# Performance work log

Measured on AMD Instinct MI355X. Metric: run time of the kernel, lower is better.

Reference implementation:

```python
import jax, jax.numpy as jnp
from jax import lax
import numpy as np

D_MODEL = 1024
D_STATE = 64
D_CONV = 4
EXPAND = 2
HEADDIM = 64
D_INNER = EXPAND * D_MODEL          # 2048
NHEADS = D_INNER // HEADDIM         # 32
CHUNK = 64
CONV_DIM = D_INNER + 2 * D_STATE    # 2176
D_IN_PROJ = 2 * D_INNER + 2 * D_STATE + NHEADS  # 4256
B_SZ = 4
SEQLEN = 2048
EPS = 1e-5


def _silu(x):
    return x * jax.nn.sigmoid(x)


def _segsum(x):
    # x: [..., T]; returns [..., T, T] with [i,j] = sum_{j<k<=i} x[k], -inf above diag
    T = x.shape[-1]
    xe = jnp.broadcast_to(x[..., None], x.shape + (T,))
    strict_lower = jnp.tril(jnp.ones((T, T), bool), -1)
    xe = jnp.where(strict_lower, xe, 0.0)
    s = jnp.cumsum(xe, axis=-2)
    lower = jnp.tril(jnp.ones((T, T), bool), 0)
    return jnp.where(lower, s, -jnp.inf)


def setup_inputs() -> dict:
    key = jax.random.key(0)
    ks = jax.random.split(key, 5)
    u = jax.random.normal(ks[0], (B_SZ, SEQLEN, D_MODEL), jnp.float32)
    W_in = jax.random.normal(ks[1], (D_IN_PROJ, D_MODEL), jnp.float32) * 0.02
    conv_w = jax.random.normal(ks[2], (CONV_DIM, 1, D_CONV), jnp.float32) * 0.2  # depthwise kernel
    conv_b = jnp.zeros((CONV_DIM,), jnp.float32)
    dt_bias = jax.random.uniform(ks[3], (NHEADS,), jnp.float32, -1.0, 1.0)
    A_log = jnp.log(jnp.linspace(1.0, float(NHEADS), NHEADS)).astype(jnp.float32)
    D = jnp.ones((NHEADS,), jnp.float32)
    norm_w = jnp.ones((D_INNER,), jnp.float32)
    W_out = jax.random.normal(ks[4], (D_MODEL, D_INNER), jnp.float32) * 0.02
    return dict(u=u, W_in=W_in, conv_w=conv_w, conv_b=conv_b, dt_bias=dt_bias,
                A_log=A_log, D=D, norm_w=norm_w, W_out=W_out)


def reference(u, W_in, conv_w, conv_b, dt_bias, A_log, D, norm_w, W_out):
    b, s, _ = u.shape
    A = -jnp.exp(A_log)                                   # [H]
    zxbcdt = u @ W_in.T                                   # [b,s,D_IN_PROJ]
    z = zxbcdt[..., :D_INNER]
    xBC = zxbcdt[..., D_INNER:D_INNER + CONV_DIM]
    dt = jax.nn.softplus(zxbcdt[..., D_INNER + CONV_DIM:] + dt_bias)  # [b,s,H]

    # causal depthwise conv1d (left pad d_conv-1 == torch pad-both + slice[:s])
    xc = lax.conv_general_dilated(
        xBC.transpose(0, 2, 1), conv_w, window_strides=(1,),
        padding=[(D_CONV - 1, 0)], feature_group_count=CONV_DIM,
        dimension_numbers=('NCH', 'OIH', 'NCH'))
    xBC = _silu(xc.transpose(0, 2, 1) + conv_b)           # [b,s,CONV_DIM]

    x = xBC[..., :D_INNER].reshape(b, s, NHEADS, HEADDIM)
    Bm = xBC[..., D_INNER:D_INNER + D_STATE]              # [b,s,N]
    Cm = xBC[..., D_INNER + D_STATE:]                     # [b,s,N]

    # SSD chunked scan
    nch = s // CHUNK
    xs = (x * dt[..., None]).reshape(b, nch, CHUNK, NHEADS, HEADDIM)
    Ad = (A * dt).reshape(b, nch, CHUNK, NHEADS)
    Br = Bm.reshape(b, nch, CHUNK, D_STATE)
    Cr = Cm.reshape(b, nch, CHUNK, D_STATE)
    A_ch = Ad.transpose(0, 1, 3, 2)                       # [b,c,h,l]
    A_cum = jnp.cumsum(A_ch, axis=-1)
    L = jnp.exp(_segsum(A_ch))                            # [b,c,h,l,l]
    Y_diag = jnp.einsum('bcln,bcsn,bchls,bcshp->bclhp', Cr, Br, L, xs)
    decay_states = jnp.exp(A_cum[..., -1:] - A_cum)       # [b,c,h,l]
    states = jnp.einsum('bchl,bcln,bclhp->bchpn', decay_states, Br, xs)
    init = jnp.zeros((b, 1, NHEADS, HEADDIM, D_STATE), xs.dtype)
    states = jnp.concatenate([init, states], axis=1)      # [b,c+1,h,p,n]
    total_decay = jnp.pad(A_cum[..., -1].transpose(0, 2, 1), ((0, 0), (0, 0), (1, 0)))
    decay_chunk = jnp.exp(_segsum(total_decay))           # [b,h,c+1,c+1]
    new_states = jnp.einsum('bhzc,bchpn->bzhpn', decay_chunk, states)
    states = new_states[:, :-1]                           # [b,c,h,p,n]
    state_decay_out = jnp.exp(A_cum)
    Y_off = jnp.einsum('bcln,bchpn,bchl->bclhp', Cr, states, state_decay_out)
    y = (Y_diag + Y_off).reshape(b, s, NHEADS, HEADDIM)

    y = y + x * D[:, None]
    y = y.reshape(b, s, D_INNER)
    # gated RMSNorm
    y = y * _silu(z)
    y = y * lax.rsqrt(jnp.mean(y * y, axis=-1, keepdims=True) + EPS) * norm_w
    return y @ W_out.T
```

## Files before the change

### kernel.cpp

```cpp
#include <hip/hip_runtime.h>
#include <hip/hip_bf16.h>

#define BSZ 4
#define SEQ 2048
#define DMODEL 1024
#define DINNER 2048
#define DSTATE 64
#define NH 32
#define HD 64
#define CKL 64
#define NCH 32
#define CONVD 2176
#define DPROJ 4256
#define N1 4224
#define MTOT 8192
#define YSTR 72

typedef __hip_bfloat16 bf16;
typedef __attribute__((ext_vector_type(8))) short short8;
typedef __attribute__((ext_vector_type(4))) short short4_;
typedef __attribute__((ext_vector_type(4))) float f32x4;

__device__ __forceinline__ float sigmoidf_(float x) { return 1.0f / (1.0f + __expf(-x)); }
__device__ __forceinline__ float bits2f(short s) { return __uint_as_float(((unsigned)(unsigned short)s) << 16); }
__device__ __forceinline__ short f2bits(float f) {
    bf16 h = __float2bfloat16(f);
    return *reinterpret_cast<short*>(&h);
}

__device__ __forceinline__ void gl_lds16(const bf16* g, bf16* l) {
    __builtin_amdgcn_global_load_lds((const __attribute__((address_space(1))) void*)g,
                                     (__attribute__((address_space(3))) void*)l, 16, 0, 0);
}

__device__ __forceinline__ f32x4 MF(short8 a, short8 b, f32x4 c) {
    return __builtin_amdgcn_mfma_f32_16x16x32_bf16(a, b, c, 0, 0, 0);
}

template<int N> __device__ __forceinline__ void vmw() {
    if constexpr (N == 0)      asm volatile("s_waitcnt vmcnt(0)" ::: "memory");
    else if constexpr (N == 3) asm volatile("s_waitcnt vmcnt(3)" ::: "memory");
    else if constexpr (N == 6) asm volatile("s_waitcnt vmcnt(6)" ::: "memory");
    else                       asm volatile("s_waitcnt vmcnt(15)" ::: "memory");
}

__device__ __forceinline__ void swzx(int& bx, int& by) {
    int nx = gridDim.x;
    int nwg = nx * gridDim.y;
    int Lr = blockIdx.y * nx + blockIdx.x;
    int L = (Lr & 7) * (nwg >> 3) + (Lr >> 3);
    int GSZ = nx * 8;
    int g = L / GSZ, r = L - g * GSZ;
    bx = r % nx;
    by = g * 8 + r / nx;
}

__global__ void k_cvt2(const float* __restrict__ W_in, const float* __restrict__ W_out,
                       const float* __restrict__ nw, bf16* __restrict__ win_b,
                       bf16* __restrict__ wout_b) {
    int g = (blockIdx.x * 256 + threadIdx.x) * 4;
    if (g < N1 * DMODEL) {
        f32x4 f = *(const f32x4*)&W_in[g];
        short4_ o;
#pragma unroll
        for (int j = 0; j < 4; j++) o[j] = f2bits(f[j]);
        *(short4_*)&win_b[g] = o;
    } else if (g < N1 * DMODEL + DMODEL * DINNER) {
        int g2 = g - N1 * DMODEL;
        f32x4 f = *(const f32x4*)&W_out[g2];
        f32x4 w = *(const f32x4*)&nw[g2 & (DINNER - 1)];
        short4_ o;
#pragma unroll
        for (int j = 0; j < 4; j++) o[j] = f2bits(f[j] * w[j]);
        *(short4_*)&wout_b[g2] = o;
    }
}

#define BARWAIT()                                           \
    __builtin_amdgcn_s_barrier();                           \
    asm volatile("s_waitcnt lgkmcnt(0)" ::: "memory");      \
    __builtin_amdgcn_sched_barrier(0);                      \
    __builtin_amdgcn_s_setprio(1)
#define ENDPH()                                             \
    __builtin_amdgcn_s_setprio(0);                          \
    __builtin_amdgcn_s_barrier()

__global__ __launch_bounds__(512, 2) void k_g1(const bf16* __restrict__ Ap,
                                               const bf16* __restrict__ Wp,
                                               bf16* __restrict__ Cp) {
    __shared__ __align__(16) short sA[2][16384];
    __shared__ __align__(16) short sB[2][12288];
    const int tid = threadIdx.x;
    const int lane = tid & 63, w = tid >> 6;
    const int wm = w >> 2, wn = w & 3;
    const int lr = lane & 15, lk = lane >> 4;
    int bx, by; swzx(bx, by);
    const int m0 = by * 256, n0 = bx * 192;
    const int ld = DMODEL;

    const int r8 = tid >> 3;
    const int c8 = ((tid & 7) ^ (r8 & 7)) * 8;
    const bf16* pA = Ap + (size_t)(m0 + r8) * ld + c8;
    const bf16* pB = Wp + (size_t)(n0 + r8) * ld + c8;

    auto stA = [&](int d, int t) {
#pragma unroll
        for (int h = 0; h < 2; h++)
// ... 185 lines not shown
        __builtin_amdgcn_s_barrier();
        rb = (rb == 2) ? 0 : rb + 1;
        sb = (sb == 2) ? 0 : sb + 1;
    }
#undef RDA2
#undef RDB2
#undef MM2
#undef SSQ2

#pragma unroll
    for (int im = 0; im < 4; im++) {
        float s = ssq[im];
        s += __shfl_down(s, 32);
        s += __shfl_down(s, 16);
        if (lane < 16) rsrow[wm * 64 + im * 16 + lane] = rsqrtf(s * (1.0f / DINNER) + 1e-5f);
    }
    __syncthreads();
#pragma unroll
    for (int im = 0; im < 4; im++) {
        int rl = wm * 64 + im * 16 + lk * 4;
        int row = m0 + rl;
#pragma unroll
        for (int rr = 0; rr < 4; rr++) {
            float s = rsrow[rl + rr];
#pragma unroll
            for (int jn = 0; jn < 4; jn++) {
                int col = n0 + wn * 64 + jn * 16 + lr;
                Cp[(size_t)(row + rr) * DMODEL + col] = acc[im][jn][rr] * s;
            }
        }
    }
}

__global__ __launch_bounds__(256) void k_prep(const float* __restrict__ u, const float* __restrict__ W_in,
                                              const float* __restrict__ dt_bias,
                                              bf16* __restrict__ u_b, float* __restrict__ dtt) {
    __shared__ __align__(16) float us[8 * DMODEL];
    const int t0 = blockIdx.x * 8;
    const int tid = threadIdx.x;
    const float* ur = u + (size_t)t0 * DMODEL;
    bf16* ub = u_b + (size_t)t0 * DMODEL;
#pragma unroll
    for (int i = 0; i < 8; i++) {
        int idx = (i * 256 + tid) * 4;
        f32x4 v = *(const f32x4*)&ur[idx];
        *(f32x4*)&us[idx] = v;
        short4_ o;
#pragma unroll
        for (int j = 0; j < 4; j++) o[j] = f2bits(v[j]);
        *(short4_*)&ub[idx] = o;
    }
    __syncthreads();
    const int h = tid >> 3, sub = tid & 7;
    const float* wr = W_in + (size_t)(DPROJ - NH + h) * DMODEL;
    float s[8] = {};
    for (int k = sub * 4; k < DMODEL; k += 32) {
        f32x4 w4 = *(const f32x4*)&wr[k];
#pragma unroll
        for (int rr = 0; rr < 8; rr++) {
            const float* up = &us[rr * DMODEL + k];
            s[rr] += up[0] * w4[0] + up[1] * w4[1] + up[2] * w4[2] + up[3] * w4[3];
        }
    }
#pragma unroll
    for (int rr = 0; rr < 8; rr++) {
        s[rr] += __shfl_down(s[rr], 4, 8);
        s[rr] += __shfl_down(s[rr], 2, 8);
        s[rr] += __shfl_down(s[rr], 1, 8);
    }
    if (sub == 0) {
        float bh = dt_bias[h];
#pragma unroll
        for (int rr = 0; rr < 8; rr++) {
            float x = s[rr] + bh;
            dtt[(size_t)h * MTOT + t0 + rr] = (x > 20.f) ? x : log1pf(__expf(x));
        }
    }
}

__global__ void k_conv(const bf16* __restrict__ zx, const float* __restrict__ cw,
                       const float* __restrict__ cb, bf16* __restrict__ xbc) {
    int g = (blockIdx.x * 256 + threadIdx.x) * 4;
    if (g >= MTOT * CONVD) return;
    int c0 = g % CONVD;
    int t = g / CONVD;
    int s = t & (SEQ - 1);
    const short* base = (const short*)(zx + (size_t)t * N1 + DINNER + c0);
    f32x4 w0 = *(const f32x4*)&cw[(c0 + 0) * 4];
    f32x4 w1 = *(const f32x4*)&cw[(c0 + 1) * 4];
    f32x4 w2 = *(const f32x4*)&cw[(c0 + 2) * 4];
    f32x4 w3 = *(const f32x4*)&cw[(c0 + 3) * 4];
    f32x4 a = *(const f32x4*)&cb[c0];
#pragma unroll
    for (int k = 0; k < 4; k++) {
        int st = s - 3 + k;
        if (st >= 0) {
            short4_ v = *(const short4_*)(base + (long)(k - 3) * N1);
            a[0] += bits2f(v[0]) * w0[k];
            a[1] += bits2f(v[1]) * w1[k];
            a[2] += bits2f(v[2]) * w2[k];
            a[3] += bits2f(v[3]) * w3[k];
        }
    }
    short4_ o;
#pragma unroll
    for (int j = 0; j < 4; j++) o[j] = f2bits(a[j] * sigmoidf_(a[j]));
    *(short4_*)&xbc[g] = o;
}

__global__ __launch_bounds__(256) void k_ssd(const bf16* __restrict__ xbc, const float* __restrict__ dtt,
                                             const float* __restrict__ A_log, const float* __restrict__ Dp,
                                             bf16* __restrict__ zx) {
    __shared__ __align__(16) short Ct[2][64 * YSTR];
    __shared__ __align__(16) short Bt[2][64 * YSTR];
    __shared__ __align__(16) short Bn[2][64 * YSTR];
    __shared__ __align__(16) short Xt[2][32 * YSTR];
    __shared__ __align__(16) short Sb[2][32 * YSTR];
    __shared__ __align__(16) short Gs[4 * 16 * YSTR];
    __shared__ __align__(16) float Sf[32 * 68];
    __shared__ __align__(16) float sdt2[2][64], sAc2[2][64], sf2[2][64];
    __shared__ float set2[2];

    const int ph = blockIdx.x, h = blockIdx.y, b = blockIdx.z;
    const int tid = threadIdx.x;
    const int lane = tid & 63, w = tid >> 6;
    const int lr = lane & 15, lk = lane >> 4;
    const float Ah = -__expf(A_log[h]);
    const float Dh = Dp[h];
    const int xcol = h * HD + ph * 32;

    const int lrow = tid >> 2, c0 = (tid & 3) * 16, px = (tid & 3) * 8;
    const int zl = 16 * w + (lane >> 2), zp = (lane & 3) * 8;

    short8 rC0, rC1, rB0, rB1, rX, rZ;
    float rdt;
    auto load_chunk = [&](int cc) {
        int rows0 = b * SEQ + cc * CKL;
        const short* rp = (const short*)(xbc + (size_t)(rows0 + lrow) * CONVD);
        rC0 = *(const short8*)&rp[DINNER + DSTATE + c0];
        rC1 = *(const short8*)&rp[DINNER + DSTATE + c0 + 8];
        rB0 = *(const short8*)&rp[DINNER + c0];
        rB1 = *(const short8*)&rp[DINNER + c0 + 8];
        rX  = *(const short8*)&rp[xcol + px];
        rZ  = *(const short8*)((const short*)zx + (size_t)(rows0 + zl) * N1 + xcol + zp);
        rdt = dtt[(size_t)h * MTOT + rows0 + lane];
    };
    auto scatter = [&](int buf) {
        *(short8*)&Ct[buf][lrow * YSTR + c0] = rC0;
        *(short8*)&Ct[buf][lrow * YSTR + c0 + 8] = rC1;
        *(short8*)&Bt[buf][lrow * YSTR + c0] = rB0;
        *(short8*)&Bt[buf][lrow * YSTR + c0 + 8] = rB1;
#pragma unroll
        for (int j = 0; j < 8; j++) {
            Bn[buf][(c0 + j) * YSTR + lrow] = rB0[j];
            Bn[buf][(c0 + 8 + j) * YSTR + lrow] = rB1[j];
            Xt[buf][(px + j) * YSTR + lrow] = rX[j];
        }
    };
    auto dtscan = [&](int buf) {
        if (tid < 64) {
            float dv = rdt;
            float v = Ah * dv;
#pragma unroll
            for (int d = 1; d < 64; d <<= 1) { float o = __shfl_up(v, d); if (tid >= d) v += o; }
            float tot = __shfl(v, 63);
            sdt2[buf][tid] = dv; sAc2[buf][tid] = v; sf2[buf][tid] = __expf(tot - v) * dv;
            if (tid == 63) set2[buf] = __expf(tot);
        }
    };

    for (int i = tid; i < 32 * 68; i += 256) Sf[i] = 0.f;
    for (int i = tid; i < 32 * YSTR; i += 256) Sb[0][i] = 0;
    load_chunk(0);
    scatter(0);
    dtscan(0);
    __syncthreads();

    for (int c = 0; c < NCH; c++) {
        const int par = c & 1, nb = par ^ 1;
        const int rows0 = b * SEQ + c * CKL;
        float etot = set2[par];
        short8 zcur = rZ;
        if (c + 1 < NCH) load_chunk(c + 1);

        short8 cf0 = *(const short8*)&Ct[par][(16 * w + lr) * YSTR + lk * 8];
        short8 cf1 = *(const short8*)&Ct[par][(16 * w + lr) * YSTR + 32 + lk * 8];
        f32x4 acc[2];
#pragma unroll
        for (int t = 0; t < 2; t++) {
            short8 s0 = *(const short8*)&Sb[par][(16 * t + lr) * YSTR + lk * 8];
            short8 s1 = *(const short8*)&Sb[par][(16 * t + lr) * YSTR + 32 + lk * 8];
            acc[t] = __builtin_amdgcn_mfma_f32_16x16x32_bf16(cf0, s0, (f32x4){0.f, 0.f, 0.f, 0.f}, 0, 0, 0);
            acc[t] = __builtin_amdgcn_mfma_f32_16x16x32_bf16(cf1, s1, acc[t], 0, 0, 0);
        }
        float sAcl[4], el[4];
#pragma unroll
        for (int rr = 0; rr < 4; rr++) { sAcl[rr] = sAc2[par][16 * w + lk * 4 + rr]; el[rr] = __expf(sAcl[rr]); }
#pragma unroll
        for (int t = 0; t < 2; t++)
#pragma unroll
            for (int rr = 0; rr < 4; rr++) acc[t][rr] *= el[rr];
        short* gw = Gs + w * 16 * YSTR;
#pragma unroll
        for (int t = 0; t < 4; t++) {
            short8 b0 = *(const short8*)&Bt[par][(16 * t + lr) * YSTR + lk * 8];
            short8 b1 = *(const short8*)&Bt[par][(16 * t + lr) * YSTR + 32 + lk * 8];
            f32x4 g = __builtin_amdgcn_mfma_f32_16x16x32_bf16(cf0, b0, (f32x4){0.f, 0.f, 0.f, 0.f}, 0, 0, 0);
            g = __builtin_amdgcn_mfma_f32_16x16x32_bf16(cf1, b1, g, 0, 0, 0);
            int s = 16 * t + lr;
            float sAcs = sAc2[par][s], dts = sdt2[par][s];
#pragma unroll
            for (int rr = 0; rr < 4; rr++) {
                int l = 16 * w + lk * 4 + rr;
                float v = (s <= l) ? g[rr] * __expf(sAcl[rr] - sAcs) * dts : 0.f;
                gw[(lk * 4 + rr) * YSTR + s] = f2bits(v);
            }
        }
        short8 gf0 = *(const short8*)&gw[lr * YSTR + lk * 8];
        short8 gf1 = *(const short8*)&gw[lr * YSTR + 32 + lk * 8];
#pragma unroll
        for (int t = 0; t < 2; t++) {
            short8 x0 = *(const short8*)&Xt[par][(16 * t + lr) * YSTR + lk * 8];
            short8 x1 = *(const short8*)&Xt[par][(16 * t + lr) * YSTR + 32 + lk * 8];
            acc[t] = __builtin_amdgcn_mfma_f32_16x16x32_bf16(gf0, x0, acc[t], 0, 0, 0);
            acc[t] = __builtin_amdgcn_mfma_f32_16x16x32_bf16(gf1, x1, acc[t], 0, 0, 0);
        }
        {
            int pw = w & 1, nh2 = w >> 1;
            short8 xt0 = *(const short8*)&Xt[par][(16 * pw + lr) * YSTR + lk * 8];
            short8 xt1 = *(const short8*)&Xt[par][(16 * pw + lr) * YSTR + 32 + lk * 8];
            f32x4 sa0 = *(const f32x4*)&sf2[par][lk * 8];
            f32x4 sa1 = *(const f32x4*)&sf2[par][lk * 8 + 4];
            f32x4 sb0 = *(const f32x4*)&sf2[par][32 + lk * 8];
            f32x4 sb1 = *(const f32x4*)&sf2[par][32 + lk * 8 + 4];
            short8 xd0, xd1;
#pragma unroll
            for (int j = 0; j < 4; j++) {
                xd0[j]     = f2bits(bits2f(xt0[j])     * sa0[j]);
                xd0[4 + j] = f2bits(bits2f(xt0[4 + j]) * sa1[j]);
                xd1[j]     = f2bits(bits2f(xt1[j])     * sb0[j]);
                xd1[4 + j] = f2bits(bits2f(xt1[4 + j]) * sb1[j]);
            }
#pragma unroll
            for (int j = 0; j < 2; j++) {
                int nt = 2 * nh2 + j;
                short8 b0 = *(const short8*)&Bn[par][(16 * nt + lr) * YSTR + lk * 8];
                short8 b1 = *(const short8*)&Bn[par][(16 * nt + lr) * YSTR + 32 + lk * 8];
                f32x4 sacc = __builtin_amdgcn_mfma_f32_16x16x32_bf16(xd0, b0, (f32x4){0.f, 0.f, 0.f, 0.f}, 0, 0, 0);
                sacc = __builtin_amdgcn_mfma_f32_16x16x32_bf16(xd1, b1, sacc, 0, 0, 0);
#pragma unroll
                for (int rr = 0; rr < 4; rr++) {
                    int n = 16 * nt + lr;
                    int p = 16 * pw + lk * 4 + rr;
                    float nv = Sf[p * 68 + n] * etot + sacc[rr];
                    Sf[p * 68 + n] = nv;
                    Sb[nb][p * YSTR + n] = f2bits(nv);
                }
            }
        }
#pragma unroll
        for (int t = 0; t < 2; t++) {
#pragma unroll
            for (int rr = 0; rr < 4; rr++) {
                int p = 16 * t + lr;
                int l = 16 * w + lk * 4 + rr;
                float y = acc[t][rr] + Dh * bits2f(Xt[par][p * YSTR + l]);
                Ct[par][l * YSTR + p] = f2bits(y);
            }
        }
        {
            short8 y8 = *(const short8*)&Ct[par][zl * YSTR + zp];
            short* zpp = (short*)zx + (size_t)(rows0 + zl) * N1 + xcol + zp;
            short8 o;
#pragma unroll
            for (int j = 0; j < 8; j++) {
                float z = bits2f(zcur[j]);
                o[j] = f2bits(bits2f(y8[j]) * (z * sigmoidf_(z)));
            }
            *(short8*)zpp = o;
        }
        if (c + 1 < NCH) {
            scatter(nb);
            dtscan(nb);
        }
        __syncthreads();
    }
}

extern "C" void kernel_launch(void* const* d_in, const int* in_sizes, int n_in,
                              void* d_out, int out_size, void* d_ws, size_t ws_size,
                              hipStream_t stream) {
    const float* u       = (const float*)d_in[0];
    const float* W_in    = (const float*)d_in[1];
    const float* conv_w  = (const float*)d_in[2];
    const float* conv_b  = (const float*)d_in[3];
    const float* dt_bias = (const float*)d_in[4];
    const float* A_log   = (const float*)d_in[5];
    const float* Dp      = (const float*)d_in[6];
    const float* norm_w  = (const float*)d_in[7];
    const float* W_out   = (const float*)d_in[8];
    float* out = (float*)d_out;

    char* ws = (char*)d_ws;
    bf16* zx     = (bf16*)ws;  ws += (size_t)MTOT * N1 * 2;
    bf16* xbc    = (bf16*)ws;  ws += (size_t)MTOT * CONVD * 2;
    bf16* wout_b = (bf16*)ws;  ws += (size_t)DMODEL * DINNER * 2;
    float* dtt   = (float*)ws; ws += (size_t)NH * MTOT * 4;

    bf16* u_b   = (bf16*)d_out;
    bf16* win_b = (bf16*)((char*)d_out + (size_t)MTOT * DMODEL * 2);

    k_prep<<<MTOT / 8, 256, 0, stream>>>(u, W_in, dt_bias, u_b, dtt);
    k_cvt2<<<((N1 * DMODEL + DMODEL * DINNER) / 4 + 255) / 256, 256, 0, stream>>>(
        W_in, W_out, norm_w, win_b, wout_b);

    k_g1<<<dim3(N1 / 192, MTOT / 256), 512, 0, stream>>>(u_b, win_b, zx);

    k_conv<<<(MTOT * CONVD / 4 + 255) / 256, 256, 0, stream>>>(zx, conv_w, conv_b, xbc);

    k_ssd<<<dim3(2, NH, BSZ), 256, 0, stream>>>(xbc, dtt, A_log, Dp, zx);

    k_g2<<<dim3(DMODEL / 128, MTOT / 256), 512, 0, stream>>>(zx, wout_b, out);
}
```

Before: 390.8 us.

## Single-buffer SSD chunk tiles in LDS to fit two blocks per CU

The k_ssd kernel drops double buffering of the C, B, B-transposed and X tiles in shared memory, keeping only one copy plus an extra barrier before the next chunk is scattered in. It also adds a launch bound that asks for two blocks per CU. The aim is to cut LDS use so more blocks can be resident and hide latency. The cost is an extra __syncthreads per chunk and less overlap between the scatter and compute. The dt projection loop also switches to a vectorized 16-byte LDS load.

New measurement: 391.7 us. Within noise of the previous version (+0.2%).

```diff
diff --git a/kernel.cpp b/kernel.cpp
--- a/kernel.cpp
+++ b/kernel.cpp
@@ -350,8 +350,8 @@
         f32x4 w4 = *(const f32x4*)&wr[k];
 #pragma unroll
         for (int rr = 0; rr < 8; rr++) {
-            const float* up = &us[rr * DMODEL + k];
-            s[rr] += up[0] * w4[0] + up[1] * w4[1] + up[2] * w4[2] + up[3] * w4[3];
+            f32x4 u4 = *(const f32x4*)&us[rr * DMODEL + k];
+            s[rr] += u4[0] * w4[0] + u4[1] * w4[1] + u4[2] * w4[2] + u4[3] * w4[3];
         }
     }
 #pragma unroll
@@ -400,13 +400,13 @@
     *(short4_*)&xbc[g] = o;
 }
 
-__global__ __launch_bounds__(256) void k_ssd(const bf16* __restrict__ xbc, const float* __restrict__ dtt,
-                                             const float* __restrict__ A_log, const float* __restrict__ Dp,
-                                             bf16* __restrict__ zx) {
-    __shared__ __align__(16) short Ct[2][64 * YSTR];
-    __shared__ __align__(16) short Bt[2][64 * YSTR];
-    __shared__ __align__(16) short Bn[2][64 * YSTR];
-    __shared__ __align__(16) short Xt[2][32 * YSTR];
+__global__ __launch_bounds__(256, 2) void k_ssd(const bf16* __restrict__ xbc, const float* __restrict__ dtt,
+                                                const float* __restrict__ A_log, const float* __restrict__ Dp,
+                                                bf16* __restrict__ zx) {
+    __shared__ __align__(16) short Ct[64 * YSTR];
+    __shared__ __align__(16) short Bt[64 * YSTR];
+    __shared__ __align__(16) short Bn[64 * YSTR];
+    __shared__ __align__(16) short Xt[32 * YSTR];
     __shared__ __align__(16) short Sb[2][32 * YSTR];
     __shared__ __align__(16) short Gs[4 * 16 * YSTR];
     __shared__ __align__(16) float Sf[32 * 68];
@@ -437,16 +437,16 @@
         rZ  = *(const short8*)((const short*)zx + (size_t)(rows0 + zl) * N1 + xcol + zp);
         rdt = dtt[(size_t)h * MTOT + rows0 + lane];
     };
-    auto scatter = [&](int buf) {
-        *(short8*)&Ct[buf][lrow * YSTR + c0] = rC0;
-        *(short8*)&Ct[buf][lrow * YSTR + c0 + 8] = rC1;
-        *(short8*)&Bt[buf][lrow * YSTR + c0] = rB0;
-        *(short8*)&Bt[buf][lrow * YSTR + c0 + 8] = rB1;
+    auto scatter = [&]() {
+        *(short8*)&Ct[lrow * YSTR + c0] = rC0;
+        *(short8*)&Ct[lrow * YSTR + c0 + 8] = rC1;
+        *(short8*)&Bt[lrow * YSTR + c0] = rB0;
+        *(short8*)&Bt[lrow * YSTR + c0 + 8] = rB1;
 #pragma unroll
         for (int j = 0; j < 8; j++) {
-            Bn[buf][(c0 + j) * YSTR + lrow] = rB0[j];
-            Bn[buf][(c0 + 8 + j) * YSTR + lrow] = rB1[j];
-            Xt[buf][(px + j) * YSTR + lrow] = rX[j];
+            Bn[(c0 + j) * YSTR + lrow] = rB0[j];
+            Bn[(c0 + 8 + j) * YSTR + lrow] = rB1[j];
+            Xt[(px + j) * YSTR + lrow] = rX[j];
         }
     };
     auto dtscan = [&](int buf) {
@@ -464,7 +464,7 @@
     for (int i = tid; i < 32 * 68; i += 256) Sf[i] = 0.f;
     for (int i = tid; i < 32 * YSTR; i += 256) Sb[0][i] = 0;
     load_chunk(0);
-    scatter(0);
+    scatter();
     dtscan(0);
     __syncthreads();
 
@@ -475,8 +475,8 @@
         short8 zcur = rZ;
         if (c + 1 < NCH) load_chunk(c + 1);
 
-        short8 cf0 = *(const short8*)&Ct[par][(16 * w + lr) * YSTR + lk * 8];
-        short8 cf1 = *(const short8*)&Ct[par][(16 * w + lr) * YSTR + 32 + lk * 8];
+        short8 cf0 = *(const short8*)&Ct[(16 * w + lr) * YSTR + lk * 8];
+        short8 cf1 = *(const short8*)&Ct[(16 * w + lr) * YSTR + 32 + lk * 8];
         f32x4 acc[2];
 #pragma unroll
         for (int t = 0; t < 2; t++) {
@@ -495,8 +495,8 @@
         short* gw = Gs + w * 16 * YSTR;
 #pragma unroll
         for (int t = 0; t < 4; t++) {
-            short8 b0 = *(const short8*)&Bt[par][(16 * t + lr) * YSTR + lk * 8];
-            short8 b1 = *(const short8*)&Bt[par][(16 * t + lr) * YSTR + 32 + lk * 8];
+            short8 b0 = *(const short8*)&Bt[(16 * t + lr) * YSTR + lk * 8];
+            short8 b1 = *(const short8*)&Bt[(16 * t + lr) * YSTR + 32 + lk * 8];
             f32x4 g = __builtin_amdgcn_mfma_f32_16x16x32_bf16(cf0, b0, (f32x4){0.f, 0.f, 0.f, 0.f}, 0, 0, 0);
             g = __builtin_amdgcn_mfma_f32_16x16x32_bf16(cf1, b1, g, 0, 0, 0);
             int s = 16 * t + lr;
@@ -512,15 +512,15 @@
         short8 gf1 = *(const short8*)&gw[lr * YSTR + 32 + lk * 8];
 #pragma unroll
         for (int t = 0; t < 2; t++) {
-            short8 x0 = *(const short8*)&Xt[par][(16 * t + lr) * YSTR + lk * 8];
-            short8 x1 = *(const short8*)&Xt[par][(16 * t + lr) * YSTR + 32 + lk * 8];
+            short8 x0 = *(const short8*)&Xt[(16 * t + lr) * YSTR + lk * 8];
+            short8 x1 = *(const short8*)&Xt[(16 * t + lr) * YSTR + 32 + lk * 8];
             acc[t] = __builtin_amdgcn_mfma_f32_16x16x32_bf16(gf0, x0, acc[t], 0, 0, 0);
             acc[t] = __builtin_amdgcn_mfma_f32_16x16x32_bf16(gf1, x1, acc[t], 0, 0, 0);
         }
         {
             int pw = w & 1, nh2 = w >> 1;
-            short8 xt0 = *(const short8*)&Xt[par][(16 * pw + lr) * YSTR + lk * 8];
-            short8 xt1 = *(const short8*)&Xt[par][(16 * pw + lr) * YSTR + 32 + lk * 8];
+            short8 xt0 = *(const short8*)&Xt[(16 * pw + lr) * YSTR + lk * 8];
+            short8 xt1 = *(const short8*)&Xt[(16 * pw + lr) * YSTR + 32 + lk * 8];
             f32x4 sa0 = *(const f32x4*)&sf2[par][lk * 8];
             f32x4 sa1 = *(const f32x4*)&sf2[par][lk * 8 + 4];
             f32x4 sb0 = *(const f32x4*)&sf2[par][32 + lk * 8];
@@ -536,8 +536,8 @@
 #pragma unroll
             for (int j = 0; j < 2; j++) {
                 int nt = 2 * nh2 + j;
-                short8 b0 = *(const short8*)&Bn[par][(16 * nt + lr) * YSTR + lk * 8];
-                short8 b1 = *(const short8*)&Bn[par][(16 * nt + lr) * YSTR + 32 + lk * 8];
+                short8 b0 = *(const short8*)&Bn[(16 * nt + lr) * YSTR + lk * 8];
+                short8 b1 = *(const short8*)&Bn[(16 * nt + lr) * YSTR + 32 + lk * 8];
                 f32x4 sacc = __builtin_amdgcn_mfma_f32_16x16x32_bf16(xd0, b0, (f32x4){0.f, 0.f, 0.f, 0.f}, 0, 0, 0);
                 sacc = __builtin_amdgcn_mfma_f32_16x16x32_bf16(xd1, b1, sacc, 0, 0, 0);
 #pragma unroll
@@ -556,12 +556,12 @@
             for (int rr = 0; rr < 4; rr++) {
                 int p = 16 * t + lr;
                 int l = 16 * w + lk * 4 + rr;
-                float y = acc[t][rr] + Dh * bits2f(Xt[par][p * YSTR + l]);
-                Ct[par][l * YSTR + p] = f2bits(y);
+                float y = acc[t][rr] + Dh * bits2f(Xt[p * YSTR + l]);
+                Ct[l * YSTR + p] = f2bits(y);
             }
         }
         {
-            short8 y8 = *(const short8*)&Ct[par][zl * YSTR + zp];
+            short8 y8 = *(const short8*)&Ct[zl * YSTR + zp];
             short* zpp = (short*)zx + (size_t)(rows0 + zl) * N1 + xcol + zp;
             short8 o;
 #pragma unroll
@@ -571,8 +571,9 @@
             }
             *(short8*)zpp = o;
         }
+        __syncthreads();
         if (c + 1 < NCH) {
-            scatter(nb);
+            scatter();
             dtscan(nb);
         }
         __syncthreads();
```

## Split sequential SSD chunk scan into parallel local-state, scan, and output kernels

Applied to the files above, without the earlier changes.

Replaces the single SSD kernel, which walked all 32 chunks serially on only 256 blocks, with three kernels. The first computes per-chunk local states in parallel over 8 chunk groups, the second runs a light serial recurrence over chunk states, and the third computes the diagonal and off-diagonal outputs in parallel. Inter-chunk states are stored as bf16 in the unused xBC region of zx, and the dt cumsum moves into a separate k_dts kernel. This adds more launches and a large fp32 SL buffer in global memory, trading extra traffic for much more parallelism. It also vectorizes the u loads in k_prep.

New measurement: 396.3 us. No clear change (+1.4%).

```diff
diff --git a/kernel.cpp b/kernel.cpp
--- a/kernel.cpp
+++ b/kernel.cpp
@@ -350,8 +350,8 @@
         f32x4 w4 = *(const f32x4*)&wr[k];
 #pragma unroll
         for (int rr = 0; rr < 8; rr++) {
-            const float* up = &us[rr * DMODEL + k];
-            s[rr] += up[0] * w4[0] + up[1] * w4[1] + up[2] * w4[2] + up[3] * w4[3];
+            f32x4 u4 = *(const f32x4*)&us[rr * DMODEL + k];
+            s[rr] += u4[0] * w4[0] + u4[1] * w4[1] + u4[2] * w4[2] + u4[3] * w4[3];
         }
     }
 #pragma unroll
@@ -367,6 +367,27 @@
             float x = s[rr] + bh;
             dtt[(size_t)h * MTOT + t0 + rr] = (x > 20.f) ? x : log1pf(__expf(x));
         }
+    }
+}
+
+__global__ __launch_bounds__(256) void k_dts(const float* __restrict__ dtt, const float* __restrict__ A_log,
+                                             float* __restrict__ sAc, float* __restrict__ sfv,
+                                             float* __restrict__ etot) {
+    const int h = blockIdx.x, b = blockIdx.y;
+    const int tid = threadIdx.x, w = tid >> 6, lane = tid & 63;
+    const float Ah = -__expf(A_log[h]);
+#pragma unroll
+    for (int g = 0; g < 8; g++) {
+        int c = g * 4 + w;
+        int t0 = b * SEQ + c * CKL;
+        float dv = dtt[(size_t)h * MTOT + t0 + lane];
+        float v = Ah * dv;
+#pragma unroll
+        for (int d = 1; d < 64; d <<= 1) { float o = __shfl_up(v, d); if (lane >= d) v += o; }
+        float tot = __shfl(v, 63);
+        sAc[(size_t)h * MTOT + t0 + lane] = v;
+        sfv[(size_t)h * MTOT + t0 + lane] = __expf(tot - v) * dv;
+        if (lane == 63) etot[(h * BSZ + b) * NCH + c] = __expf(tot);
     }
 }
 
@@ -400,123 +421,44 @@
     *(short4_*)&xbc[g] = o;
 }
 
-__global__ __launch_bounds__(256) void k_ssd(const bf16* __restrict__ xbc, const float* __restrict__ dtt,
-                                             const float* __restrict__ A_log, const float* __restrict__ Dp,
-                                             bf16* __restrict__ zx) {
-    __shared__ __align__(16) short Ct[2][64 * YSTR];
-    __shared__ __align__(16) short Bt[2][64 * YSTR];
+__global__ __launch_bounds__(256, 2) void k_ssda(const bf16* __restrict__ xbc, const float* __restrict__ sfv,
+                                                 float* __restrict__ SL) {
     __shared__ __align__(16) short Bn[2][64 * YSTR];
     __shared__ __align__(16) short Xt[2][32 * YSTR];
-    __shared__ __align__(16) short Sb[2][32 * YSTR];
-    __shared__ __align__(16) short Gs[4 * 16 * YSTR];
-    __shared__ __align__(16) float Sf[32 * 68];
-    __shared__ __align__(16) float sdt2[2][64], sAc2[2][64], sf2[2][64];
-    __shared__ float set2[2];
-
-    const int ph = blockIdx.x, h = blockIdx.y, b = blockIdx.z;
+    __shared__ float sf2[2][64];
+    const int ph = blockIdx.x, h = blockIdx.y;
+    const int b = blockIdx.z >> 3, cbase = (blockIdx.z & 7) * 4;
     const int tid = threadIdx.x;
     const int lane = tid & 63, w = tid >> 6;
     const int lr = lane & 15, lk = lane >> 4;
-    const float Ah = -__expf(A_log[h]);
-    const float Dh = Dp[h];
     const int xcol = h * HD + ph * 32;
-
     const int lrow = tid >> 2, c0 = (tid & 3) * 16, px = (tid & 3) * 8;
-    const int zl = 16 * w + (lane >> 2), zp = (lane & 3) * 8;
-
-    short8 rC0, rC1, rB0, rB1, rX, rZ;
-    float rdt;
-    auto load_chunk = [&](int cc) {
+    const size_t u = (size_t)((b * NH + h) * 2 + ph);
+
+    short8 rB0, rB1, rX; float rsf;
+    auto load_grp = [&](int cc) {
         int rows0 = b * SEQ + cc * CKL;
         const short* rp = (const short*)(xbc + (size_t)(rows0 + lrow) * CONVD);
-        rC0 = *(const short8*)&rp[DINNER + DSTATE + c0];
-        rC1 = *(const short8*)&rp[DINNER + DSTATE + c0 + 8];
         rB0 = *(const short8*)&rp[DINNER + c0];
         rB1 = *(const short8*)&rp[DINNER + c0 + 8];
         rX  = *(const short8*)&rp[xcol + px];
-        rZ  = *(const short8*)((const short*)zx + (size_t)(rows0 + zl) * N1 + xcol + zp);
-        rdt = dtt[(size_t)h * MTOT + rows0 + lane];
-    };
-    auto scatter = [&](int buf) {
-        *(short8*)&Ct[buf][lrow * YSTR + c0] = rC0;
-        *(short8*)&Ct[buf][lrow * YSTR + c0 + 8] = rC1;
-        *(short8*)&Bt[buf][lrow * YSTR + c0] = rB0;
-        *(short8*)&Bt[buf][lrow * YSTR + c0 + 8] = rB1;
+        rsf = sfv[(size_t)h * MTOT + rows0 + lane];
+    };
+    auto scat = [&](int buf) {
 #pragma unroll
         for (int j = 0; j < 8; j++) {
             Bn[buf][(c0 + j) * YSTR + lrow] = rB0[j];
             Bn[buf][(c0 + 8 + j) * YSTR + lrow] = rB1[j];
             Xt[buf][(px + j) * YSTR + lrow] = rX[j];
         }
-    };
-    auto dtscan = [&](int buf) {
-        if (tid < 64) {
-            float dv = rdt;
-            float v = Ah * dv;
-#pragma unroll
-            for (int d = 1; d < 64; d <<= 1) { float o = __shfl_up(v, d); if (tid >= d) v += o; }
-            float tot = __shfl(v, 63);
-            sdt2[buf][tid] = dv; sAc2[buf][tid] = v; sf2[buf][tid] = __expf(tot - v) * dv;
-            if (tid == 63) set2[buf] = __expf(tot);
-        }
-    };
-
-    for (int i = tid; i < 32 * 68; i += 256) Sf[i] = 0.f;
-    for (int i = tid; i < 32 * YSTR; i += 256) Sb[0][i] = 0;
-    load_chunk(0);
-    scatter(0);
-    dtscan(0);
+        if (tid < 64) sf2[buf][tid] = rsf;
+    };
+
+    load_grp(cbase); scat(0);
     __syncthreads();
-
-    for (int c = 0; c < NCH; c++) {
-        const int par = c & 1, nb = par ^ 1;
-        const int rows0 = b * SEQ + c * CKL;
-        float etot = set2[par];
-        short8 zcur = rZ;
-        if (c + 1 < NCH) load_chunk(c + 1);
-
-        short8 cf0 = *(const short8*)&Ct[par][(16 * w + lr) * YSTR + lk * 8];
-        short8 cf1 = *(const short8*)&Ct[par][(16 * w + lr) * YSTR + 32 + lk * 8];
-        f32x4 acc[2];
-#pragma unroll
-        for (int t = 0; t < 2; t++) {
-            short8 s0 = *(const short8*)&Sb[par][(16 * t + lr) * YSTR + lk * 8];
-            short8 s1 = *(const short8*)&Sb[par][(16 * t + lr) * YSTR + 32 + lk * 8];
-            acc[t] = __builtin_amdgcn_mfma_f32_16x16x32_bf16(cf0, s0, (f32x4){0.f, 0.f, 0.f, 0.f}, 0, 0, 0);
-            acc[t] = __builtin_amdgcn_mfma_f32_16x16x32_bf16(cf1, s1, acc[t], 0, 0, 0);
-        }
-        float sAcl[4], el[4];
-#pragma unroll
-        for (int rr = 0; rr < 4; rr++) { sAcl[rr] = sAc2[par][16 * w + lk * 4 + rr]; el[rr] = __expf(sAcl[rr]); }
-#pragma unroll
-        for (int t = 0; t < 2; t++)
-#pragma unroll
-            for (int rr = 0; rr < 4; rr++) acc[t][rr] *= el[rr];
-        short* gw = Gs + w * 16 * YSTR;
-#pragma unroll
-        for (int t = 0; t < 4; t++) {
-            short8 b0 = *(const short8*)&Bt[par][(16 * t + lr) * YSTR + lk * 8];
-            short8 b1 = *(const short8*)&Bt[par][(16 * t + lr) * YSTR + 32 + lk * 8];
-            f32x4 g = __builtin_amdgcn_mfma_f32_16x16x32_bf16(cf0, b0, (f32x4){0.f, 0.f, 0.f, 0.f}, 0, 0, 0);
-            g = __builtin_amdgcn_mfma_f32_16x16x32_bf16(cf1, b1, g, 0, 0, 0);
-            int s = 16 * t + lr;
-            float sAcs = sAc2[par][s], dts = sdt2[par][s];
-#pragma unroll
-            for (int rr = 0; rr < 4; rr++) {
-                int l = 16 * w + lk * 4 + rr;
-                float v = (s <= l) ? g[rr] * __expf(sAcl[rr] - sAcs) * dts : 0.f;
-                gw[(lk * 4 + rr) * YSTR + s] = f2bits(v);
-            }
-        }
-        short8 gf0 = *(const short8*)&gw[lr * YSTR + lk * 8];
-        short8 gf1 = *(const short8*)&gw[lr * YSTR + 32 + lk * 8];
-#pragma unroll
-        for (int t = 0; t < 2; t++) {
-            short8 x0 = *(const short8*)&Xt[par][(16 * t + lr) * YSTR + lk * 8];
-            short8 x1 = *(const short8*)&Xt[par][(16 * t + lr) * YSTR + 32 + lk * 8];
-            acc[t] = __builtin_amdgcn_mfma_f32_16x16x32_bf16(gf0, x0, acc[t], 0, 0, 0);
-            acc[t] = __builtin_amdgcn_mfma_f32_16x16x32_bf16(gf1, x1, acc[t], 0, 0, 0);
-        }
+    for (int i = 0; i < 4; i++) {
+        const int par = i & 1, nb = par ^ 1, c = cbase + i;
+        if (i + 1 < 4) load_grp(c + 1);
         {
             int pw = w & 1, nh2 = w >> 1;
             short8 xt0 = *(const short8*)&Xt[par][(16 * pw + lr) * YSTR + lk * 8];
@@ -533,22 +475,143 @@
                 xd1[j]     = f2bits(bits2f(xt1[j])     * sb0[j]);
                 xd1[4 + j] = f2bits(bits2f(xt1[4 + j]) * sb1[j]);
             }
+            float* SLp = SL + (u * NCH + c) * (32 * 64);
 #pragma unroll
             for (int j = 0; j < 2; j++) {
                 int nt = 2 * nh2 + j;
                 short8 b0 = *(const short8*)&Bn[par][(16 * nt + lr) * YSTR + lk * 8];
                 short8 b1 = *(const short8*)&Bn[par][(16 * nt + lr) * YSTR + 32 + lk * 8];
-                f32x4 sacc = __builtin_amdgcn_mfma_f32_16x16x32_bf16(xd0, b0, (f32x4){0.f, 0.f, 0.f, 0.f}, 0, 0, 0);
-                sacc = __builtin_amdgcn_mfma_f32_16x16x32_bf16(xd1, b1, sacc, 0, 0, 0);
+                f32x4 sacc = MF(xd0, b0, (f32x4){0.f, 0.f, 0.f, 0.f});
+                sacc = MF(xd1, b1, sacc);
 #pragma unroll
                 for (int rr = 0; rr < 4; rr++) {
                     int n = 16 * nt + lr;
                     int p = 16 * pw + lk * 4 + rr;
-                    float nv = Sf[p * 68 + n] * etot + sacc[rr];
-                    Sf[p * 68 + n] = nv;
-                    Sb[nb][p * YSTR + n] = f2bits(nv);
+                    SLp[p * 64 + n] = sacc[rr];
                 }
             }
+        }
+        if (i + 1 < 4) scat(nb);
+        __syncthreads();
+    }
+}
+
+__global__ __launch_bounds__(256) void k_ssdb(const float* __restrict__ SL, const float* __restrict__ etot,
+                                              bf16* __restrict__ zx) {
+    const int u = blockIdx.x, tid = threadIdx.x;
+    const int b = u >> 6, rem = u & 63;
+    const int h = rem >> 1, ph = rem & 1;
+    float S[8];
+#pragma unroll
+    for (int j = 0; j < 8; j++) S[j] = 0.f;
+    for (int c = 0; c < NCH; c++) {
+        short8 o;
+#pragma unroll
+        for (int j = 0; j < 8; j++) o[j] = f2bits(S[j]);
+        *(short8*)((short*)zx + (size_t)(b * SEQ + c * CKL + 2 * h + ph) * N1 + DINNER + tid * 8) = o;
+        float ec = etot[(h * BSZ + b) * NCH + c];
+        const float* slp = SL + ((size_t)u * NCH + c) * (32 * 64) + tid * 8;
+        f32x4 v0 = *(const f32x4*)&slp[0];
+        f32x4 v1 = *(const f32x4*)&slp[4];
+#pragma unroll
+        for (int j = 0; j < 4; j++) { S[j] = v0[j] + ec * S[j]; S[4 + j] = v1[j] + ec * S[4 + j]; }
+    }
+}
+
+__global__ __launch_bounds__(256, 2) void k_ssdc(const bf16* __restrict__ xbc, const float* __restrict__ dtt,
+                                                 const float* __restrict__ sAc, const float* __restrict__ Dp,
+                                                 bf16* __restrict__ zx) {
+    __shared__ __align__(16) short Ct[2][64 * YSTR];
+    __shared__ __align__(16) short Bt[2][64 * YSTR];
+    __shared__ __align__(16) short Xt[2][32 * YSTR];
+    __shared__ __align__(16) short Pb[2][32 * YSTR];
+    __shared__ __align__(16) short Gs[4 * 16 * YSTR];
+    __shared__ __align__(16) float sdt2[2][64], sAc2[2][64];
+    const int ph = blockIdx.x, h = blockIdx.y;
+    const int b = blockIdx.z >> 3, cbase = (blockIdx.z & 7) * 4;
+    const int tid = threadIdx.x;
+    const int lane = tid & 63, w = tid >> 6;
+    const int lr = lane & 15, lk = lane >> 4;
+    const float Dh = Dp[h];
+    const int xcol = h * HD + ph * 32;
+    const int lrow = tid >> 2, c0 = (tid & 3) * 16, px = (tid & 3) * 8;
+    const int zl = 16 * w + (lane >> 2), zp = (lane & 3) * 8;
+
+    short8 rC0, rC1, rB0, rB1, rX, rZ, rP;
+    float rsd, rsa;
+    auto load_c = [&](int cc) {
+        int rows0 = b * SEQ + cc * CKL;
+        const short* rp = (const short*)(xbc + (size_t)(rows0 + lrow) * CONVD);
+        rC0 = *(const short8*)&rp[DINNER + DSTATE + c0];
+        rC1 = *(const short8*)&rp[DINNER + DSTATE + c0 + 8];
+        rB0 = *(const short8*)&rp[DINNER + c0];
+        rB1 = *(const short8*)&rp[DINNER + c0 + 8];
+        rX  = *(const short8*)&rp[xcol + px];
+        rZ  = *(const short8*)((const short*)zx + (size_t)(rows0 + zl) * N1 + xcol + zp);
+        rP  = *(const short8*)((const short*)zx + (size_t)(rows0 + 2 * h + ph) * N1 + DINNER + tid * 8);
+        rsd = dtt[(size_t)h * MTOT + rows0 + lane];
+        rsa = sAc[(size_t)h * MTOT + rows0 + lane];
+    };
+    auto scat = [&](int buf) {
+        *(short8*)&Ct[buf][lrow * YSTR + c0] = rC0;
+        *(short8*)&Ct[buf][lrow * YSTR + c0 + 8] = rC1;
+        *(short8*)&Bt[buf][lrow * YSTR + c0] = rB0;
+        *(short8*)&Bt[buf][lrow * YSTR + c0 + 8] = rB1;
+#pragma unroll
+        for (int j = 0; j < 8; j++) Xt[buf][(px + j) * YSTR + lrow] = rX[j];
+        *(short8*)&Pb[buf][(tid >> 3) * YSTR + (tid & 7) * 8] = rP;
+        if (tid < 64) { sdt2[buf][tid] = rsd; sAc2[buf][tid] = rsa; }
+    };
+
+    load_c(cbase); scat(0);
+    __syncthreads();
+    for (int i = 0; i < 4; i++) {
+        const int par = i & 1, nb = par ^ 1, c = cbase + i;
+        const int rows0 = b * SEQ + c * CKL;
+        short8 zcur = rZ;
+        if (i + 1 < 4) load_c(c + 1);
+
+        short8 cf0 = *(const short8*)&Ct[par][(16 * w + lr) * YSTR + lk * 8];
+        short8 cf1 = *(const short8*)&Ct[par][(16 * w + lr) * YSTR + 32 + lk * 8];
+        f32x4 acc[2];
+#pragma unroll
+        for (int t = 0; t < 2; t++) {
+            short8 s0 = *(const short8*)&Pb[par][(16 * t + lr) * YSTR + lk * 8];
+            short8 s1 = *(const short8*)&Pb[par][(16 * t + lr) * YSTR + 32 + lk * 8];
+            acc[t] = MF(cf0, s0, (f32x4){0.f, 0.f, 0.f, 0.f});
+            acc[t] = MF(cf1, s1, acc[t]);
+        }
+        float sAcl[4], el[4];
+#pragma unroll
+        for (int rr = 0; rr < 4; rr++) { sAcl[rr] = sAc2[par][16 * w + lk * 4 + rr]; el[rr] = __expf(sAcl[rr]); }
+#pragma unroll
+        for (int t = 0; t < 2; t++)
+#pragma unroll
+            for (int rr = 0; rr < 4; rr++) acc[t][rr] *= el[rr];
+        short* gw = Gs + w * 16 * YSTR;
+#pragma unroll
+        for (int t = 0; t < 4; t++) {
+            short8 b0 = *(const short8*)&Bt[par][(16 * t + lr) * YSTR + lk * 8];
+            short8 b1 = *(const short8*)&Bt[par][(16 * t + lr) * YSTR + 32 + lk * 8];
+            f32x4 g = MF(cf0, b0, (f32x4){0.f, 0.f, 0.f, 0.f});
+            g = MF(cf1, b1, g);
+            int s = 16 * t + lr;
+            float sAcs = sAc2[par][s], dts = sdt2[par][s];
+#pragma unroll
+            for (int rr = 0; rr < 4; rr++) {
+                int l = 16 * w + lk * 4 + rr;
+                float v = (s <= l) ? g[rr] * __expf(sAcl[rr] - sAcs) * dts : 0.f;
+                gw[(lk * 4 + rr) * YSTR + s] = f2bits(v);
+            }
+        }
+        short8 gf0 = *(const short8*)&gw[lr * YSTR + lk * 8];
+        short8 gf1 = *(const short8*)&gw[lr * YSTR + 32 + lk * 8];
+#pragma unroll
+        for (int t = 0; t < 2; t++) {
+            short8 x0 = *(const short8*)&Xt[par][(16 * t + lr) * YSTR + lk * 8];
+            short8 x1 = *(const short8*)&Xt[par][(16 * t + lr) * YSTR + 32 + lk * 8];
+            acc[t] = MF(gf0, x0, acc[t]);
+            acc[t] = MF(gf1, x1, acc[t]);
         }
 #pragma unroll
         for (int t = 0; t < 2; t++) {
@@ -571,10 +634,7 @@
             }
             *(short8*)zpp = o;
         }
-        if (c + 1 < NCH) {
-            scatter(nb);
-            dtscan(nb);
-        }
+        if (i + 1 < 4) scat(nb);
         __syncthreads();
     }
 }
@@ -598,11 +658,16 @@
     bf16* xbc    = (bf16*)ws;  ws += (size_t)MTOT * CONVD * 2;
     bf16* wout_b = (bf16*)ws;  ws += (size_t)DMODEL * DINNER * 2;
     float* dtt   = (float*)ws; ws += (size_t)NH * MTOT * 4;
+    float* sAcw  = (float*)ws; ws += (size_t)NH * MTOT * 4;
+    float* sfvw  = (float*)ws; ws += (size_t)NH * MTOT * 4;
+    float* etotw = (float*)ws; ws += 64 * 1024;
+    float* SL    = (float*)ws; ws += (size_t)256 * NCH * 32 * 64 * 4;
 
     bf16* u_b   = (bf16*)d_out;
     bf16* win_b = (bf16*)((char*)d_out + (size_t)MTOT * DMODEL * 2);
 
     k_prep<<<MTOT / 8, 256, 0, stream>>>(u, W_in, dt_bias, u_b, dtt);
+    k_dts<<<dim3(NH, BSZ), 256, 0, stream>>>(dtt, A_log, sAcw, sfvw, etotw);
     k_cvt2<<<((N1 * DMODEL + DMODEL * DINNER) / 4 + 255) / 256, 256, 0, stream>>>(
         W_in, W_out, norm_w, win_b, wout_b);
 
@@ -610,7 +675,9 @@
 
     k_conv<<<(MTOT * CONVD / 4 + 255) / 256, 256, 0, stream>>>(zx, conv_w, conv_b, xbc);
 
-    k_ssd<<<dim3(2, NH, BSZ), 256, 0, stream>>>(xbc, dtt, A_log, Dp, zx);
+    k_ssda<<<dim3(2, NH, BSZ * 8), 256, 0, stream>>>(xbc, sfvw, SL);
+    k_ssdb<<<256, 256, 0, stream>>>(SL, etotw, zx);
+    k_ssdc<<<dim3(2, NH, BSZ * 8), 256, 0, stream>>>(xbc, dtt, sAcw, Dp, zx);
 
     k_g2<<<dim3(DMODEL / 128, MTOT / 256), 512, 0, stream>>>(zx, wout_b, out);
 }
```

## Merge prep and weight-convert kernels; compute four timesteps per conv thread

Applied to the files above, without the earlier changes.

The u-to-bf16/dt-projection kernel and the weight-conversion kernel become a single launch, with the block index selecting which job each block does. The conv kernel now has each thread handle 4 consecutive timesteps for 4 channels, so 7 input rows are loaded instead of 16. That cuts redundant global reads of the overlapping conv window. The dt dot product reads shared memory with 16-byte vector loads, and the SSD MFMA calls go through an MF macro. The merged kernel reserves the 32KB shared buffer for every block, including the conversion blocks, which may lower their occupancy.

Result: faster. 374.4 us (-4.2%).

```diff
diff --git a/kernel.cpp b/kernel.cpp
--- a/kernel.cpp
+++ b/kernel.cpp
@@ -15,6 +15,7 @@
 #define N1 4224
 #define MTOT 8192
 #define YSTR 72
+#define CVTB 6272
 
 typedef __hip_bfloat16 bf16;
 typedef __attribute__((ext_vector_type(8))) short short8;
@@ -55,24 +56,70 @@
     by = g * 8 + r / nx;
 }
 
-__global__ void k_cvt2(const float* __restrict__ W_in, const float* __restrict__ W_out,
-                       const float* __restrict__ nw, bf16* __restrict__ win_b,
-                       bf16* __restrict__ wout_b) {
-    int g = (blockIdx.x * 256 + threadIdx.x) * 4;
-    if (g < N1 * DMODEL) {
-        f32x4 f = *(const f32x4*)&W_in[g];
+__global__ __launch_bounds__(256) void k_pre2(const float* __restrict__ u, const float* __restrict__ W_in,
+                                              const float* __restrict__ dt_bias,
+                                              const float* __restrict__ W_out, const float* __restrict__ nw,
+                                              bf16* __restrict__ u_b, float* __restrict__ dtt,
+                                              bf16* __restrict__ win_b, bf16* __restrict__ wout_b) {
+    __shared__ __align__(16) float us[8 * DMODEL];
+    const int tid = threadIdx.x;
+    if (blockIdx.x < CVTB) {
+        int g = (blockIdx.x * 256 + tid) * 4;
+        if (g < N1 * DMODEL) {
+            f32x4 f = *(const f32x4*)&W_in[g];
+            short4_ o;
+#pragma unroll
+            for (int j = 0; j < 4; j++) o[j] = f2bits(f[j]);
+            *(short4_*)&win_b[g] = o;
+        } else if (g < N1 * DMODEL + DMODEL * DINNER) {
+            int g2 = g - N1 * DMODEL;
+            f32x4 f = *(const f32x4*)&W_out[g2];
+            f32x4 w = *(const f32x4*)&nw[g2 & (DINNER - 1)];
+            short4_ o;
+#pragma unroll
+            for (int j = 0; j < 4; j++) o[j] = f2bits(f[j] * w[j]);
+            *(short4_*)&wout_b[g2] = o;
+        }
+        return;
+    }
+    const int t0 = (blockIdx.x - CVTB) * 8;
+    const float* ur = u + (size_t)t0 * DMODEL;
+    bf16* ub = u_b + (size_t)t0 * DMODEL;
+#pragma unroll
+    for (int i = 0; i < 8; i++) {
+        int idx = (i * 256 + tid) * 4;
+        f32x4 v = *(const f32x4*)&ur[idx];
+        *(f32x4*)&us[idx] = v;
         short4_ o;
 #pragma unroll
-        for (int j = 0; j < 4; j++) o[j] = f2bits(f[j]);
-        *(short4_*)&win_b[g] = o;
-    } else if (g < N1 * DMODEL + DMODEL * DINNER) {
-        int g2 = g - N1 * DMODEL;
-        f32x4 f = *(const f32x4*)&W_out[g2];
-        f32x4 w = *(const f32x4*)&nw[g2 & (DINNER - 1)];
-        short4_ o;
-#pragma unroll
-        for (int j = 0; j < 4; j++) o[j] = f2bits(f[j] * w[j]);
-        *(short4_*)&wout_b[g2] = o;
+        for (int j = 0; j < 4; j++) o[j] = f2bits(v[j]);
+        *(short4_*)&ub[idx] = o;
+    }
+    __syncthreads();
+    const int h = tid >> 3, sub = tid & 7;
+    const float* wr = W_in + (size_t)(DPROJ - NH + h) * DMODEL;
+    float s[8] = {};
+    for (int k = sub * 4; k < DMODEL; k += 32) {
+        f32x4 w4 = *(const f32x4*)&wr[k];
+#pragma unroll
+        for (int rr = 0; rr < 8; rr++) {
+            f32x4 u4 = *(const f32x4*)&us[rr * DMODEL + k];
+            s[rr] += u4[0] * w4[0] + u4[1] * w4[1] + u4[2] * w4[2] + u4[3] * w4[3];
+        }
+    }
+#pragma unroll
+    for (int rr = 0; rr < 8; rr++) {
+        s[rr] += __shfl_down(s[rr], 4, 8);
+        s[rr] += __shfl_down(s[rr], 2, 8);
+        s[rr] += __shfl_down(s[rr], 1, 8);
+    }
+    if (sub == 0) {
+        float bh = dt_bias[h];
+#pragma unroll
+        for (int rr = 0; rr < 8; rr++) {
+            float x = s[rr] + bh;
+            dtt[(size_t)h * MTOT + t0 + rr] = (x > 20.f) ? x : log1pf(__expf(x));
+        }
     }
 }
 
@@ -324,80 +371,40 @@
     }
 }
 
-__global__ __launch_bounds__(256) void k_prep(const float* __restrict__ u, const float* __restrict__ W_in,
-                                              const float* __restrict__ dt_bias,
-                                              bf16* __restrict__ u_b, float* __restrict__ dtt) {
-    __shared__ __align__(16) float us[8 * DMODEL];
-    const int t0 = blockIdx.x * 8;
-    const int tid = threadIdx.x;
-    const float* ur = u + (size_t)t0 * DMODEL;
-    bf16* ub = u_b + (size_t)t0 * DMODEL;
-#pragma unroll
-    for (int i = 0; i < 8; i++) {
-        int idx = (i * 256 + tid) * 4;
-        f32x4 v = *(const f32x4*)&ur[idx];
-        *(f32x4*)&us[idx] = v;
-        short4_ o;
-#pragma unroll
-        for (int j = 0; j < 4; j++) o[j] = f2bits(v[j]);
-        *(short4_*)&ub[idx] = o;
-    }
-    __syncthreads();
-    const int h = tid >> 3, sub = tid & 7;
-    const float* wr = W_in + (size_t)(DPROJ - NH + h) * DMODEL;
-    float s[8] = {};
-    for (int k = sub * 4; k < DMODEL; k += 32) {
-        f32x4 w4 = *(const f32x4*)&wr[k];
-#pragma unroll
-        for (int rr = 0; rr < 8; rr++) {
-            const float* up = &us[rr * DMODEL + k];
-            s[rr] += up[0] * w4[0] + up[1] * w4[1] + up[2] * w4[2] + up[3] * w4[3];
-        }
-    }
-#pragma unroll
-    for (int rr = 0; rr < 8; rr++) {
-        s[rr] += __shfl_down(s[rr], 4, 8);
-        s[rr] += __shfl_down(s[rr], 2, 8);
-        s[rr] += __shfl_down(s[rr], 1, 8);
-    }
-    if (sub == 0) {
-        float bh = dt_bias[h];
-#pragma unroll
-        for (int rr = 0; rr < 8; rr++) {
-            float x = s[rr] + bh;
-            dtt[(size_t)h * MTOT + t0 + rr] = (x > 20.f) ? x : log1pf(__expf(x));
-        }
-    }
-}
-
-__global__ void k_conv(const bf16* __restrict__ zx, const float* __restrict__ cw,
-                       const float* __restrict__ cb, bf16* __restrict__ xbc) {
-    int g = (blockIdx.x * 256 + threadIdx.x) * 4;
-    if (g >= MTOT * CONVD) return;
-    int c0 = g % CONVD;
-    int t = g / CONVD;
-    int s = t & (SEQ - 1);
-    const short* base = (const short*)(zx + (size_t)t * N1 + DINNER + c0);
+__global__ __launch_bounds__(256) void k_conv(const bf16* __restrict__ zx, const float* __restrict__ cw,
+                                              const float* __restrict__ cb, bf16* __restrict__ xbc) {
+    const int g = blockIdx.x * 256 + threadIdx.x;
+    const int c0 = (g % 544) * 4;
+    const int t0 = (g / 544) * 4;
+    const int s0 = t0 & (SEQ - 1);
+    const short* base = (const short*)(zx + (size_t)t0 * N1 + DINNER + c0);
     f32x4 w0 = *(const f32x4*)&cw[(c0 + 0) * 4];
     f32x4 w1 = *(const f32x4*)&cw[(c0 + 1) * 4];
     f32x4 w2 = *(const f32x4*)&cw[(c0 + 2) * 4];
     f32x4 w3 = *(const f32x4*)&cw[(c0 + 3) * 4];
-    f32x4 a = *(const f32x4*)&cb[c0];
-#pragma unroll
-    for (int k = 0; k < 4; k++) {
-        int st = s - 3 + k;
-        if (st >= 0) {
-            short4_ v = *(const short4_*)(base + (long)(k - 3) * N1);
-            a[0] += bits2f(v[0]) * w0[k];
-            a[1] += bits2f(v[1]) * w1[k];
-            a[2] += bits2f(v[2]) * w2[k];
-            a[3] += bits2f(v[3]) * w3[k];
-        }
-    }
-    short4_ o;
-#pragma unroll
-    for (int j = 0; j < 4; j++) o[j] = f2bits(a[j] * sigmoidf_(a[j]));
-    *(short4_*)&xbc[g] = o;
+    f32x4 bias = *(const f32x4*)&cb[c0];
+    short4_ v[7];
+#pragma unroll
+    for (int o = 0; o < 7; o++) {
+        if (s0 + o - 3 >= 0) v[o] = *(const short4_*)(base + (long)(o - 3) * N1);
+        else v[o] = (short4_){0, 0, 0, 0};
+    }
+#pragma unroll
+    for (int j = 0; j < 4; j++) {
+        f32x4 a = bias;
+#pragma unroll
+        for (int k = 0; k < 4; k++) {
+            short4_ x = v[j + k];
+            a[0] += bits2f(x[0]) * w0[k];
+            a[1] += bits2f(x[1]) * w1[k];
+            a[2] += bits2f(x[2]) * w2[k];
+            a[3] += bits2f(x[3]) * w3[k];
+        }
+        short4_ o_;
+#pragma unroll
+        for (int jj = 0; jj < 4; jj++) o_[jj] = f2bits(a[jj] * sigmoidf_(a[jj]));
+        *(short4_*)((short*)xbc + (size_t)(t0 + j) * CONVD + c0) = o_;
+    }
 }
 
 __global__ __launch_bounds__(256) void k_ssd(const bf16* __restrict__ xbc, const float* __restrict__ dtt,
@@ -482,8 +489,8 @@
         for (int t = 0; t < 2; t++) {
             short8 s0 = *(const short8*)&Sb[par][(16 * t + lr) * YSTR + lk * 8];
             short8 s1 = *(const short8*)&Sb[par][(16 * t + lr) * YSTR + 32 + lk * 8];
-            acc[t] = __builtin_amdgcn_mfma_f32_16x16x32_bf16(cf0, s0, (f32x4){0.f, 0.f, 0.f, 0.f}, 0, 0, 0);
-            acc[t] = __builtin_amdgcn_mfma_f32_16x16x32_bf16(cf1, s1, acc[t], 0, 0, 0);
+            acc[t] = MF(cf0, s0, (f32x4){0.f, 0.f, 0.f, 0.f});
+            acc[t] = MF(cf1, s1, acc[t]);
         }
         float sAcl[4], el[4];
 #pragma unroll
@@ -497,8 +504,8 @@
         for (int t = 0; t < 4; t++) {
             short8 b0 = *(const short8*)&Bt[par][(16 * t + lr) * YSTR + lk * 8];
             short8 b1 = *(const short8*)&Bt[par][(16 * t + lr) * YSTR + 32 + lk * 8];
-            f32x4 g = __builtin_amdgcn_mfma_f32_16x16x32_bf16(cf0, b0, (f32x4){0.f, 0.f, 0.f, 0.f}, 0, 0, 0);
-            g = __builtin_amdgcn_mfma_f32_16x16x32_bf16(cf1, b1, g, 0, 0, 0);
+            f32x4 g = MF(cf0, b0, (f32x4){0.f, 0.f, 0.f, 0.f});
+            g = MF(cf1, b1, g);
             int s = 16 * t + lr;
             float sAcs = sAc2[par][s], dts = sdt2[par][s];
 #pragma unroll
@@ -514,8 +521,8 @@
         for (int t = 0; t < 2; t++) {
             short8 x0 = *(const short8*)&Xt[par][(16 * t + lr) * YSTR + lk * 8];
             short8 x1 = *(const short8*)&Xt[par][(16 * t + lr) * YSTR + 32 + lk * 8];
-            acc[t] = __builtin_amdgcn_mfma_f32_16x16x32_bf16(gf0, x0, acc[t], 0, 0, 0);
-            acc[t] = __builtin_amdgcn_mfma_f32_16x16x32_bf16(gf1, x1, acc[t], 0, 0, 0);
+            acc[t] = MF(gf0, x0, acc[t]);
+            acc[t] = MF(gf1, x1, acc[t]);
         }
         {
             int pw = w & 1, nh2 = w >> 1;
@@ -538,8 +545,8 @@
                 int nt = 2 * nh2 + j;
                 short8 b0 = *(const short8*)&Bn[par][(16 * nt + lr) * YSTR + lk * 8];
                 short8 b1 = *(const short8*)&Bn[par][(16 * nt + lr) * YSTR + 32 + lk * 8];
-                f32x4 sacc = __builtin_amdgcn_mfma_f32_16x16x32_bf16(xd0, b0, (f32x4){0.f, 0.f, 0.f, 0.f}, 0, 0, 0);
-                sacc = __builtin_amdgcn_mfma_f32_16x16x32_bf16(xd1, b1, sacc, 0, 0, 0);
+                f32x4 sacc = MF(xd0, b0, (f32x4){0.f, 0.f, 0.f, 0.f});
+                sacc = MF(xd1, b1, sacc);
 #pragma unroll
                 for (int rr = 0; rr < 4; rr++) {
                     int n = 16 * nt + lr;
@@ -602,13 +609,12 @@
     bf16* u_b   = (bf16*)d_out;
     bf16* win_b = (bf16*)((char*)d_out + (size_t)MTOT * DMODEL * 2);
 
-    k_prep<<<MTOT / 8, 256, 0, stream>>>(u, W_in, dt_bias, u_b, dtt);
-    k_cvt2<<<((N1 * DMODEL + DMODEL * DINNER) / 4 + 255) / 256, 256, 0, stream>>>(
-        W_in, W_out, norm_w, win_b, wout_b);
+    k_pre2<<<CVTB + MTOT / 8, 256, 0, stream>>>(u, W_in, dt_bias, W_out, norm_w,
+                                                u_b, dtt, win_b, wout_b);
 
     k_g1<<<dim3(N1 / 192, MTOT / 256), 512, 0, stream>>>(u_b, win_b, zx);
 
-    k_conv<<<(MTOT * CONVD / 4 + 255) / 256, 256, 0, stream>>>(zx, conv_w, conv_b, xbc);
+    k_conv<<<(MTOT / 4) * (CONVD / 4) / 256, 256, 0, stream>>>(zx, conv_w, conv_b, xbc);
 
     k_ssd<<<dim3(2, NH, BSZ), 256, 0, stream>>>(xbc, dtt, A_log, Dp, zx);
 
```
